# Kernel optimization log

Measured on AMD Instinct MI355X. Metric: run time of the kernel, lower is better.

The kernel has to match this reference:

```python
import jax, jax.numpy as jnp
import numpy as np

B, TQ, TV, D = 8, 2048, 2048, 128
NEG = 1e9  # keras Attention uses additive -1e9 masking for fp32


def setup_inputs() -> dict:
    key = jax.random.key(0)
    kq, kv, kk, kmq, kmv = jax.random.split(key, 5)
    q = jax.random.normal(kq, (B, TQ, D), dtype=jnp.float32)
    v = jax.random.normal(kv, (B, TV, D), dtype=jnp.float32)
    k = jax.random.normal(kk, (B, TV, D), dtype=jnp.float32)
    # learned scalar scale from use_scale=True, initialized to ones
    scale = jnp.ones((), dtype=jnp.float32)
    mask_q = jax.random.randint(kmq, (B, TQ), 0, 2) > 0
    mask_v = jax.random.randint(kmv, (B, TV), 0, 2) > 0
    return {"q": q, "v": v, "k": k, "scale": scale, "mask_q": mask_q, "mask_v": mask_v}


def reference(q, v, k, scale, mask_q, mask_v):
    # scores: [B, Tq, Tv]
    scores = scale * jnp.einsum('bqd,bkd->bqk', q, k)
    # key/value mask: additive -1e9 on masked positions (keras semantics)
    scores = scores - NEG * (1.0 - mask_v[:, None, :].astype(scores.dtype))
    weights = jax.nn.softmax(scores, axis=-1)
    out = jnp.einsum('bqk,bkd->bqd', weights, v)
    # query mask zeroes out masked query rows
    out = out * mask_q[:, :, None].astype(out.dtype)
    return out
```

## Files before the change

kernel.cpp:

```cpp
#include <hip/hip_runtime.h>
#include <cstddef>

#define NB 8
#define TQ 2048
#define TV 2048
#define DD 128
#define KVT 32
#define NWV 4
#define CHW (TV / NWV)
#define NT  (CHW / KVT)

typedef _Float16 f16x8 __attribute__((ext_vector_type(8)));
typedef _Float16 f16x4 __attribute__((ext_vector_type(4)));
typedef float f32x4 __attribute__((ext_vector_type(4)));

template <int CTRL>
__device__ __forceinline__ float dpp_mov(float x) {
  return __builtin_bit_cast(float,
      __builtin_amdgcn_update_dpp(0, __builtin_bit_cast(int, x), CTRL, 0xF, 0xF, true));
}
__device__ __forceinline__ float rowmax16(float x) {
  x = fmaxf(x, dpp_mov<0x128>(x));
  x = fmaxf(x, dpp_mov<0x124>(x));
  x = fmaxf(x, dpp_mov<0x122>(x));
  x = fmaxf(x, dpp_mov<0x121>(x));
  return x;
}

__global__ __launch_bounds__(256) void prepass_kernel(
    const float* __restrict__ q, const float* __restrict__ k,
    const float* __restrict__ v, const float* __restrict__ scale_p,
    _Float16* __restrict__ qh, _Float16* __restrict__ kh2, _Float16* __restrict__ vt2)
{
  __shared__ _Float16 tlds[32 * 34];
  const int tid = threadIdx.x;
  const int bid = blockIdx.x;
  if (bid < 2048) {
    const float sc = scale_p[0];
    size_t idx = (size_t)bid * 256 + tid;
    float4 x = ((const float4*)q)[idx];
    f16x4 h; h[0] = (_Float16)(sc * x.x); h[1] = (_Float16)(sc * x.y);
    h[2] = (_Float16)(sc * x.z); h[3] = (_Float16)(sc * x.w);
    ((f16x4*)qh)[idx] = h;
  } else if (bid < 2048 + 512) {
    int tb = bid - 2048;
    int b = tb >> 6, kt = tb & 63;
    int row = tid >> 3, d0 = (tid & 7) * 4;
    const float* src = k + ((size_t)(b * TV + kt * 32 + row)) * DD;
    _Float16* dst = kh2 + ((size_t)(b * 64 + kt)) * 4096;
#pragma unroll
    for (int it = 0; it < 4; ++it) {
      float4 x = *(const float4*)(src + it * 32 + d0);
      f16x4 h; h[0] = (_Float16)x.x; h[1] = (_Float16)x.y;
      h[2] = (_Float16)x.z; h[3] = (_Float16)x.w;
      *(f16x4*)(dst + it * 1024 + row * 32 + d0) = h;
    }
  } else {
    int tb = bid - 2048 - 512;
    int b = tb >> 8, rem = tb & 255;
    int kt = rem >> 2, dt = rem & 3;
    int r = tid >> 3, c0 = (tid & 7) * 4;
    float4 x = *(const float4*)&v[((size_t)b * TV + kt * 32 + r) * DD + dt * 32 + c0];
    tlds[(c0 + 0) * 34 + r] = (_Float16)x.x;
    tlds[(c0 + 1) * 34 + r] = (_Float16)x.y;
    tlds[(c0 + 2) * 34 + r] = (_Float16)x.z;
    tlds[(c0 + 3) * 34 + r] = (_Float16)x.w;
    __syncthreads();
    int dl = tid >> 3, k0 = (tid & 7) * 4;
    f16x4 h;
#pragma unroll
    for (int i = 0; i < 4; ++i) h[i] = tlds[dl * 34 + k0 + i];
    size_t eidx = (((size_t)b * 64 + kt) * 128 + (dt * 32 + dl)) * 32 + k0;
    *(f16x4*)&vt2[eidx] = h;
  }
}

__global__ __launch_bounds__(256, 2) void attn_main(
    const _Float16* __restrict__ qh, const _Float16* __restrict__ kh2,
    const _Float16* __restrict__ vt2,
    const int* __restrict__ mask_q, const int* __restrict__ mask_v,
    float* __restrict__ out)
{
  __shared__ __align__(16) _Float16 plds_all[NWV][2][16 * 40];
  __shared__ __align__(16) float osh[32 * 132];
  __shared__ float msh[NWV][32], lsh[NWV][32];

  const int tid = threadIdx.x;
  const int w = tid >> 6;
  const int lane = tid & 63;
  const int l15 = lane & 15, lg = lane >> 4;

  const int b = blockIdx.x & 7;
  const int qg = blockIdx.x >> 3;
  const int qbase = qg * 32;

  const _Float16* qhb = qh + ((size_t)b * TQ + qbase) * DD;
  const _Float16* ktiles = kh2 + (size_t)b * 64 * 4096;
  const _Float16* vtiles = vt2 + (size_t)b * 64 * 4096;
  const int* mvb = mask_v + b * TV;

  f16x8 qf[2][4];
#pragma unroll
  for (int rb = 0; rb < 2; ++rb)
#pragma unroll
    for (int kc = 0; kc < 4; ++kc)
      qf[rb][kc] = *(const f16x8*)(qhb + (size_t)(rb * 16 + l15) * DD + kc * 32 + lg * 8);

  f16x8 vones;
#pragma unroll
  for (int j = 0; j < 8; ++j) vones[j] = (_Float16)1.f;

  f32x4 acc[2][8];
  f32x4 accl[2];
#pragma unroll
  for (int rb = 0; rb < 2; ++rb) {
    accl[rb] = (f32x4){0.f, 0.f, 0.f, 0.f};
#pragma unroll
    for (int ct = 0; ct < 8; ++ct) acc[rb][ct] = (f32x4){0.f, 0.f, 0.f, 0.f};
  }
  float m[2][4];
#pragma unroll
  for (int rb = 0; rb < 2; ++rb)
#pragma unroll
    for (int r = 0; r < 4; ++r) m[rb][r] = -3.0e38f;

  const int tbase = w * NT;

  f16x8 ka[8], kb[8];

  {
    const _Float16* kt0 = ktiles + (size_t)tbase * 4096;
#pragma unroll
    for (int kc = 0; kc < 4; ++kc) {
      ka[2 * kc]     = *(const f16x8*)(kt0 + kc * 1024 + l15 * 32 + lg * 8);
      ka[2 * kc + 1] = *(const f16x8*)(kt0 + kc * 1024 + (16 + l15) * 32 + lg * 8);
    }
  }

  auto step = [&](int tile, f16x8 (&kcur)[8], f16x8 (&kpre)[8], int tilep) {
    const _Float16* ktbp = ktiles + (size_t)tilep * 4096;
#pragma unroll
    for (int kc = 0; kc < 4; ++kc) {
      kpre[2 * kc]     = *(const f16x8*)(ktbp + kc * 1024 + l15 * 32 + lg * 8);
      kpre[2 * kc + 1] = *(const f16x8*)(ktbp + kc * 1024 + (16 + l15) * 32 + lg * 8);
    }
    const _Float16* vtb = vtiles + (size_t)tile * 4096;
    f16x8 vfr[8];
#pragma unroll
    for (int ct = 0; ct < 8; ++ct)
      vfr[ct] = *(const f16x8*)(vtb + (ct * 16 + l15) * 32 + lg * 8);
    const int kt = tile * KVT;
    const float a0 = (mvb[kt + l15]      != 0) ? 0.f : -1e9f;
    const float a1 = (mvb[kt + 16 + l15] != 0) ? 0.f : -1e9f;

    f32x4 s[2][2];
    s[0][0] = (f32x4){0,0,0,0}; s[0][1] = (f32x4){0,0,0,0};
    s[1][0] = (f32x4){0,0,0,0}; s[1][1] = (f32x4){0,0,0,0};
    __builtin_amdgcn_s_setprio(1);
#pragma unroll
    for (int kc = 0; kc < 4; ++kc) {
      s[0][0] = __builtin_amdgcn_mfma_f32_16x16x32_f16(qf[0][kc], kcur[2*kc],   s[0][0], 0, 0, 0);
      s[1][0] = __builtin_amdgcn_mfma_f32_16x16x32_f16(qf[1][kc], kcur[2*kc],   s[1][0], 0, 0, 0);
      s[0][1] = __builtin_amdgcn_mfma_f32_16x16x32_f16(qf[0][kc], kcur[2*kc+1], s[0][1], 0, 0, 0);
      s[1][1] = __builtin_amdgcn_mfma_f32_16x16x32_f16(qf[1][kc], kcur[2*kc+1], s[1][1], 0, 0, 0);
    }
    __builtin_amdgcn_s_setprio(0);

    f16x8 pa[2];
#pragma unroll
    for (int rb = 0; rb < 2; ++rb) {
      float pmx[4];
      bool grow = false;
#pragma unroll
      for (int r = 0; r < 4; ++r) {
        s[rb][0][r] += a0;
        s[rb][1][r] += a1;
        pmx[r] = rowmax16(fmaxf(s[rb][0][r], s[rb][1][r]));
        grow = grow || (pmx[r] > m[rb][r] + 8.f);
      }
      if (__any(grow)) {
        f32x4 alv;
#pragma unroll
        for (int r = 0; r < 4; ++r) {
          float mn = fmaxf(m[rb][r], pmx[r]);
          alv[r] = __expf(m[rb][r] - mn);
          m[rb][r] = mn;
        }
        accl[rb] *= alv;
#pragma unroll
        for (int ct = 0; ct < 8; ++ct) acc[rb][ct] *= alv;
      }
      _Float16* pl = plds_all[w][rb];
#pragma unroll
      for (int r = 0; r < 4; ++r) {
        float p0 = __expf(s[rb][0][r] - m[rb][r]);
        float p1 = __expf(s[rb][1][r] - m[rb][r]);
        int row = lg * 4 + r;
        pl[row * 40 + l15]      = (_Float16)p0;
        pl[row * 40 + 16 + l15] = (_Float16)p1;
      }
      pa[rb] = *(const f16x8*)(pl + l15 * 40 + lg * 8);
    }

    __builtin_amdgcn_s_setprio(1);
#pragma unroll
    for (int ct = 0; ct < 8; ++ct) {
      acc[0][ct] = __builtin_amdgcn_mfma_f32_16x16x32_f16(pa[0], vfr[ct], acc[0][ct], 0, 0, 0);
      acc[1][ct] = __builtin_amdgcn_mfma_f32_16x16x32_f16(pa[1], vfr[ct], acc[1][ct], 0, 0, 0);
    }
    accl[0] = __builtin_amdgcn_mfma_f32_16x16x32_f16(pa[0], vones, accl[0], 0, 0, 0);
    accl[1] = __builtin_amdgcn_mfma_f32_16x16x32_f16(pa[1], vones, accl[1], 0, 0, 0);
    __builtin_amdgcn_s_setprio(0);
  };

#pragma unroll 1
  for (int t2 = 0; t2 < NT; t2 += 2) {
    step(tbase + t2,     ka, kb, tbase + t2 + 1);
    step(tbase + t2 + 1, kb, ka, (t2 + 2 < NT) ? (tbase + t2 + 2) : (tbase + t2 + 1));
  }

  if (l15 == 0) {
#pragma unroll
    for (int rb = 0; rb < 2; ++rb)
#pragma unroll
      for (int r = 0; r < 4; ++r) {
        msh[w][rb * 16 + lg * 4 + r] = m[rb][r];
        lsh[w][rb * 16 + lg * 4 + r] = accl[rb][r];
      }
  }
  __syncthreads();

  float coef[2][4];
#pragma unroll
  for (int rb = 0; rb < 2; ++rb)
#pragma unroll
    for (int r = 0; r < 4; ++r) {
      int row = rb * 16 + lg * 4 + r;
      float mstar = msh[0][row];
#pragma unroll
      for (int wv = 1; wv < NWV; ++wv) mstar = fmaxf(mstar, msh[wv][row]);
      coef[rb][r] = __expf(m[rb][r] - mstar);
    }

#pragma unroll
  for (int wv = 0; wv < NWV; ++wv) {
    if (w == wv) {
#pragma unroll
      for (int rb = 0; rb < 2; ++rb)
#pragma unroll
        for (int ct = 0; ct < 8; ++ct)
#pragma unroll
          for (int r = 0; r < 4; ++r) {
            int idx = (rb * 16 + lg * 4 + r) * 132 + ct * 16 + l15;
            float val = coef[rb][r] * acc[rb][ct][r];
            if (wv == 0) osh[idx] = val; else osh[idx] += val;
          }
    }
    __syncthreads();
  }

  {
    const int row = tid >> 3;
    const int cg = (tid & 7) * 16;
    float mstar = msh[0][row];
#pragma unroll
    for (int wv = 1; wv < NWV; ++wv) mstar = fmaxf(mstar, msh[wv][row]);
    float lstar = 0.f;
#pragma unroll
    for (int wv = 0; wv < NWV; ++wv)
      lstar += __expf(msh[wv][row] - mstar) * lsh[wv][row];
    const int qr = qbase + row;
    const float f = ((mask_q[(size_t)b * TQ + qr] != 0) ? 1.f : 0.f) / lstar;
    float* orow = out + ((size_t)b * TQ + qr) * DD + cg;
#pragma unroll
    for (int i4 = 0; i4 < 4; ++i4) {
      float4 p = *(float4*)&osh[row * 132 + cg + i4 * 4];
      float4 o; o.x = p.x * f; o.y = p.y * f; o.z = p.z * f; o.w = p.w * f;
      *(float4*)(orow + i4 * 4) = o;
    }
  }
}

__global__ __launch_bounds__(64, 4) void attn_f32_kernel(
    const float* __restrict__ q, const float* __restrict__ v,
    const float* __restrict__ k, const float* __restrict__ scale_p,
    const int* __restrict__ mask_q, const int* __restrict__ mask_v,
    float* __restrict__ out)
{
  __shared__ __align__(16) _Float16 plds[16 * 40];
  const int lane = threadIdx.x & 63;
  const int l15 = lane & 15, lg = lane >> 4;
  const int qblocks = TQ / 16;
  const int b = blockIdx.x / qblocks, qb = blockIdx.x % qblocks;
  const int qbase = qb * 16;
  const float scale = scale_p[0];
  const float* qp = q + ((size_t)b * TQ + qbase) * DD;
  const float* kbase = k + (size_t)b * TV * DD;
  const float* vbase = v + (size_t)b * TV * DD;
  const int* mvb = mask_v + b * TV;
  f16x8 qf[4];
#pragma unroll
  for (int kc = 0; kc < 4; ++kc) {
    float4 a = *(const float4*)(qp + (size_t)l15 * DD + kc * 32 + lg * 8);
    float4 bb = *(const float4*)(qp + (size_t)l15 * DD + kc * 32 + lg * 8 + 4);
    f16x8 h; h[0]=(_Float16)a.x;h[1]=(_Float16)a.y;h[2]=(_Float16)a.z;h[3]=(_Float16)a.w;
    h[4]=(_Float16)bb.x;h[5]=(_Float16)bb.y;h[6]=(_Float16)bb.z;h[7]=(_Float16)bb.w;
    qf[kc]=h;
  }
  f32x4 acc[8];
#pragma unroll
  for (int i = 0; i < 8; ++i) acc[i] = (f32x4){0.f,0.f,0.f,0.f};
  float m[4], lsum[4];
#pragma unroll
  for (int r = 0; r < 4; ++r) { m[r] = -3.0e38f; lsum[r] = 0.f; }
  for (int kt = 0; kt < TV; kt += KVT) {
    f32x4 s0 = {0,0,0,0}, s1 = {0,0,0,0};
#pragma unroll
    for (int kc = 0; kc < 4; ++kc) {
      const float* kp0 = kbase + (size_t)(kt + l15) * DD + kc * 32 + lg * 8;
      float4 a = *(const float4*)kp0; float4 bb = *(const float4*)(kp0 + 4);
      f16x8 kf0; kf0[0]=(_Float16)a.x;kf0[1]=(_Float16)a.y;kf0[2]=(_Float16)a.z;kf0[3]=(_Float16)a.w;
      kf0[4]=(_Float16)bb.x;kf0[5]=(_Float16)bb.y;kf0[6]=(_Float16)bb.z;kf0[7]=(_Float16)bb.w;
      s0 = __builtin_amdgcn_mfma_f32_16x16x32_f16(qf[kc], kf0, s0, 0, 0, 0);
      const float* kp1 = kbase + (size_t)(kt + 16 + l15) * DD + kc * 32 + lg * 8;
      a = *(const float4*)kp1; bb = *(const float4*)(kp1 + 4);
      f16x8 kf1; kf1[0]=(_Float16)a.x;kf1[1]=(_Float16)a.y;kf1[2]=(_Float16)a.z;kf1[3]=(_Float16)a.w;
      kf1[4]=(_Float16)bb.x;kf1[5]=(_Float16)bb.y;kf1[6]=(_Float16)bb.z;kf1[7]=(_Float16)bb.w;
      s1 = __builtin_amdgcn_mfma_f32_16x16x32_f16(qf[kc], kf1, s1, 0, 0, 0);
    }
    const float a0 = (mvb[kt + l15] != 0) ? 0.f : -1e9f;
    const float a1 = (mvb[kt + 16 + l15] != 0) ? 0.f : -1e9f;
    float pmx[4];
#pragma unroll
    for (int r = 0; r < 4; ++r) {
      s0[r] = s0[r] * scale + a0; s1[r] = s1[r] * scale + a1;
      pmx[r] = fmaxf(s0[r], s1[r]);
    }
#pragma unroll
    for (int off = 1; off < 16; off <<= 1)
#pragma unroll
      for (int r = 0; r < 4; ++r) pmx[r] = fmaxf(pmx[r], __shfl_xor(pmx[r], off, 64));
    float al[4], ps[4];
#pragma unroll
    for (int r = 0; r < 4; ++r) {
      float mn = fmaxf(m[r], pmx[r]);
      al[r] = __expf(m[r] - mn); m[r] = mn;
      float p0 = __expf(s0[r] - mn), p1 = __expf(s1[r] - mn);
      ps[r] = p0 + p1;
      int row = lg * 4 + r;
      plds[row * 40 + l15] = (_Float16)p0;
      plds[row * 40 + 16 + l15] = (_Float16)p1;
    }
#pragma unroll
    for (int off = 1; off < 16; off <<= 1)
#pragma unroll
      for (int r = 0; r < 4; ++r) ps[r] += __shfl_xor(ps[r], off, 64);
#pragma unroll
    for (int r = 0; r < 4; ++r) {
      lsum[r] = lsum[r] * al[r] + ps[r];
#pragma unroll
      for (int ct = 0; ct < 8; ++ct) acc[ct][r] *= al[r];
    }
    f16x8 pa = *(const f16x8*)&plds[l15 * 40 + lg * 8];
#pragma unroll
    for (int ct = 0; ct < 8; ++ct) {
      const float* vp = vbase + (size_t)(kt + lg * 8) * DD + ct * 16 + l15;
      f16x8 vfx;
#pragma unroll
      for (int j = 0; j < 8; ++j) vfx[j] = (_Float16)vp[(size_t)j * DD];
      acc[ct] = __builtin_amdgcn_mfma_f32_16x16x32_f16(pa, vfx, acc[ct], 0, 0, 0);
    }
  }
  const int* mqb = mask_q + b * TQ;
#pragma unroll
  for (int r = 0; r < 4; ++r) {
    int row = lg * 4 + r;
    int qr = qbase + row;
    float f = ((mqb[qr] != 0) ? 1.f : 0.f) / lsum[r];
    float* orow = out + ((size_t)b * TQ + qr) * DD;
#pragma unroll
    for (int ct = 0; ct < 8; ++ct) orow[ct * 16 + l15] = acc[ct][r] * f;
  }
}

extern "C" void kernel_launch(void* const* d_in, const int* in_sizes, int n_in,
                              void* d_out, int out_size, void* d_ws, size_t ws_size,
                              hipStream_t stream) {
  const float* q      = (const float*)d_in[0];
  const float* v      = (const float*)d_in[1];
  const float* k      = (const float*)d_in[2];
  const float* scale  = (const float*)d_in[3];
  const int*   mask_q = (const int*)d_in[4];
  const int*   mask_v = (const int*)d_in[5];
  float* out = (float*)d_out;

  const size_t need = 3ull * NB * TV * DD * sizeof(_Float16);
  if (ws_size >= need) {
    _Float16* qh  = (_Float16*)d_ws;
    _Float16* kh2 = qh + (size_t)NB * TQ * DD;
    _Float16* vt2 = kh2 + (size_t)NB * TV * DD;
    hipLaunchKernelGGL(prepass_kernel, dim3(2048 + 512 + 2048), dim3(256), 0, stream,
                       q, k, v, scale, qh, kh2, vt2);
    hipLaunchKernelGGL(attn_main, dim3(NB * (TQ / 32)), dim3(256), 0, stream,
                       qh, kh2, vt2, mask_q, mask_v, out);
  } else {
    hipLaunchKernelGGL(attn_f32_kernel, dim3(NB * (TQ / 16)), dim3(64), 0, stream,
                       q, v, k, scale, mask_q, mask_v, out);
  }
}
```

Before: 56.55 us.

## Fuse Q conversion into attention kernel, use exp2 softmax and precomputed mask biases

Drops the Q fp32-to-fp16 prepass and has the attention kernel load fp32 Q and convert it, with the scale and log2(e) folded in, so the qh workspace round trip goes away. Softmax switches from __expf to the hardware exp2 builtin. Mask biases are precomputed per tile as packed fp16 values in registers. The lazy-rescale row max is now taken only when a rescale triggers, using a larger threshold, and the K/V loop is fully unrolled with single-buffered prefetch of the next K and V. The larger rescale threshold and the fp16 -60000 mask bias change numeric headroom, and full unrolling raises register pressure.

After: 56.38 us. About the same (-0.3%).

```diff
diff --git a/kernel.cpp b/kernel.cpp
--- a/kernel.cpp
+++ b/kernel.cpp
@@ -9,10 +9,15 @@
 #define NWV 4
 #define CHW (TV / NWV)
 #define NT  (CHW / KVT)
+#define LOG2E 1.4426950408889634f
 
 typedef _Float16 f16x8 __attribute__((ext_vector_type(8)));
 typedef _Float16 f16x4 __attribute__((ext_vector_type(4)));
 typedef float f32x4 __attribute__((ext_vector_type(4)));
+
+__device__ __forceinline__ float fast_exp2(float x) {
+  return __builtin_amdgcn_exp2f(x);
+}
 
 template <int CTRL>
 __device__ __forceinline__ float dpp_mov(float x) {
@@ -28,23 +33,14 @@
 }
 
 __global__ __launch_bounds__(256) void prepass_kernel(
-    const float* __restrict__ q, const float* __restrict__ k,
-    const float* __restrict__ v, const float* __restrict__ scale_p,
-    _Float16* __restrict__ qh, _Float16* __restrict__ kh2, _Float16* __restrict__ vt2)
+    const float* __restrict__ k, const float* __restrict__ v,
+    _Float16* __restrict__ kh2, _Float16* __restrict__ vt2)
 {
   __shared__ _Float16 tlds[32 * 34];
   const int tid = threadIdx.x;
   const int bid = blockIdx.x;
-  if (bid < 2048) {
-    const float sc = scale_p[0];
-    size_t idx = (size_t)bid * 256 + tid;
-    float4 x = ((const float4*)q)[idx];
-    f16x4 h; h[0] = (_Float16)(sc * x.x); h[1] = (_Float16)(sc * x.y);
-    h[2] = (_Float16)(sc * x.z); h[3] = (_Float16)(sc * x.w);
-    ((f16x4*)qh)[idx] = h;
-  } else if (bid < 2048 + 512) {
-    int tb = bid - 2048;
-    int b = tb >> 6, kt = tb & 63;
+  if (bid < 512) {
+    int b = bid >> 6, kt = bid & 63;
     int row = tid >> 3, d0 = (tid & 7) * 4;
     const float* src = k + ((size_t)(b * TV + kt * 32 + row)) * DD;
     _Float16* dst = kh2 + ((size_t)(b * 64 + kt)) * 4096;
@@ -56,7 +52,7 @@
       *(f16x4*)(dst + it * 1024 + row * 32 + d0) = h;
     }
   } else {
-    int tb = bid - 2048 - 512;
+    int tb = bid - 512;
     int b = tb >> 8, rem = tb & 255;
     int kt = rem >> 2, dt = rem & 3;
     int r = tid >> 3, c0 = (tid & 7) * 4;
@@ -76,8 +72,8 @@
 }
 
 __global__ __launch_bounds__(256, 2) void attn_main(
-    const _Float16* __restrict__ qh, const _Float16* __restrict__ kh2,
-    const _Float16* __restrict__ vt2,
+    const float* __restrict__ q, const float* __restrict__ scale_p,
+    const _Float16* __restrict__ kh2, const _Float16* __restrict__ vt2,
     const int* __restrict__ mask_q, const int* __restrict__ mask_v,
     float* __restrict__ out)
 {
@@ -93,18 +89,37 @@
   const int b = blockIdx.x & 7;
   const int qg = blockIdx.x >> 3;
   const int qbase = qg * 32;
-
-  const _Float16* qhb = qh + ((size_t)b * TQ + qbase) * DD;
+  const int kv0 = w * CHW;
+
   const _Float16* ktiles = kh2 + (size_t)b * 64 * 4096;
   const _Float16* vtiles = vt2 + (size_t)b * 64 * 4096;
   const int* mvb = mask_v + b * TV;
 
+  const float sc2 = scale_p[0] * LOG2E;
   f16x8 qf[2][4];
 #pragma unroll
   for (int rb = 0; rb < 2; ++rb)
 #pragma unroll
-    for (int kc = 0; kc < 4; ++kc)
-      qf[rb][kc] = *(const f16x8*)(qhb + (size_t)(rb * 16 + l15) * DD + kc * 32 + lg * 8);
+    for (int kc = 0; kc < 4; ++kc) {
+      const float* qp = q + ((size_t)b * TQ + qbase + rb * 16 + l15) * DD + kc * 32 + lg * 8;
+      float4 xa = *(const float4*)qp;
+      float4 xb = *(const float4*)(qp + 4);
+      f16x8 h;
+      h[0] = (_Float16)(sc2 * xa.x); h[1] = (_Float16)(sc2 * xa.y);
+      h[2] = (_Float16)(sc2 * xa.z); h[3] = (_Float16)(sc2 * xa.w);
+      h[4] = (_Float16)(sc2 * xb.x); h[5] = (_Float16)(sc2 * xb.y);
+      h[6] = (_Float16)(sc2 * xb.z); h[7] = (_Float16)(sc2 * xb.w);
+      qf[rb][kc] = h;
+    }
+
+  const unsigned short HBIAS = __builtin_bit_cast(unsigned short, (_Float16)(-60000.0f));
+  unsigned mbp[NT];
+#pragma unroll
+  for (int t = 0; t < NT; ++t) {
+    unsigned h0 = (mvb[kv0 + t * KVT + l15]      != 0) ? 0u : (unsigned)HBIAS;
+    unsigned h1 = (mvb[kv0 + t * KVT + 16 + l15] != 0) ? 0u : (unsigned)HBIAS;
+    mbp[t] = h0 | (h1 << 16);
+  }
 
   f16x8 vones;
 #pragma unroll
@@ -126,32 +141,23 @@
 
   const int tbase = w * NT;
 
-  f16x8 ka[8], kb[8];
-
+  f16x8 kbuf[8], vbuf[8];
   {
-    const _Float16* kt0 = ktiles + (size_t)tbase * 4096;
+    const _Float16* ktb = ktiles + (size_t)tbase * 4096;
 #pragma unroll
     for (int kc = 0; kc < 4; ++kc) {
-      ka[2 * kc]     = *(const f16x8*)(kt0 + kc * 1024 + l15 * 32 + lg * 8);
-      ka[2 * kc + 1] = *(const f16x8*)(kt0 + kc * 1024 + (16 + l15) * 32 + lg * 8);
-    }
-  }
-
-  auto step = [&](int tile, f16x8 (&kcur)[8], f16x8 (&kpre)[8], int tilep) {
-    const _Float16* ktbp = ktiles + (size_t)tilep * 4096;
-#pragma unroll
-    for (int kc = 0; kc < 4; ++kc) {
-      kpre[2 * kc]     = *(const f16x8*)(ktbp + kc * 1024 + l15 * 32 + lg * 8);
-      kpre[2 * kc + 1] = *(const f16x8*)(ktbp + kc * 1024 + (16 + l15) * 32 + lg * 8);
-    }
-    const _Float16* vtb = vtiles + (size_t)tile * 4096;
-    f16x8 vfr[8];
+      kbuf[2 * kc]     = *(const f16x8*)(ktb + kc * 1024 + l15 * 32 + lg * 8);
+      kbuf[2 * kc + 1] = *(const f16x8*)(ktb + kc * 1024 + (16 + l15) * 32 + lg * 8);
+    }
+    const _Float16* vtb = vtiles + (size_t)tbase * 4096;
 #pragma unroll
     for (int ct = 0; ct < 8; ++ct)
-      vfr[ct] = *(const f16x8*)(vtb + (ct * 16 + l15) * 32 + lg * 8);
-    const int kt = tile * KVT;
-    const float a0 = (mvb[kt + l15]      != 0) ? 0.f : -1e9f;
-    const float a1 = (mvb[kt + 16 + l15] != 0) ? 0.f : -1e9f;
+      vbuf[ct] = *(const f16x8*)(vtb + (ct * 16 + l15) * 32 + lg * 8);
+  }
+
+#pragma unroll
+  for (int t = 0; t < NT; ++t) {
+    const int tile = tbase + t;
 
     f32x4 s[2][2];
     s[0][0] = (f32x4){0,0,0,0}; s[0][1] = (f32x4){0,0,0,0};
@@ -159,31 +165,43 @@
     __builtin_amdgcn_s_setprio(1);
 #pragma unroll
     for (int kc = 0; kc < 4; ++kc) {
-      s[0][0] = __builtin_amdgcn_mfma_f32_16x16x32_f16(qf[0][kc], kcur[2*kc],   s[0][0], 0, 0, 0);
-      s[1][0] = __builtin_amdgcn_mfma_f32_16x16x32_f16(qf[1][kc], kcur[2*kc],   s[1][0], 0, 0, 0);
-      s[0][1] = __builtin_amdgcn_mfma_f32_16x16x32_f16(qf[0][kc], kcur[2*kc+1], s[0][1], 0, 0, 0);
-      s[1][1] = __builtin_amdgcn_mfma_f32_16x16x32_f16(qf[1][kc], kcur[2*kc+1], s[1][1], 0, 0, 0);
+      s[0][0] = __builtin_amdgcn_mfma_f32_16x16x32_f16(qf[0][kc], kbuf[2*kc],   s[0][0], 0, 0, 0);
+      s[1][0] = __builtin_amdgcn_mfma_f32_16x16x32_f16(qf[1][kc], kbuf[2*kc],   s[1][0], 0, 0, 0);
+      s[0][1] = __builtin_amdgcn_mfma_f32_16x16x32_f16(qf[0][kc], kbuf[2*kc+1], s[0][1], 0, 0, 0);
+      s[1][1] = __builtin_amdgcn_mfma_f32_16x16x32_f16(qf[1][kc], kbuf[2*kc+1], s[1][1], 0, 0, 0);
     }
     __builtin_amdgcn_s_setprio(0);
 
+    if (t + 1 < NT) {
+      const _Float16* ktb = ktiles + (size_t)(tile + 1) * 4096;
+#pragma unroll
+      for (int kc = 0; kc < 4; ++kc) {
+        kbuf[2 * kc]     = *(const f16x8*)(ktb + kc * 1024 + l15 * 32 + lg * 8);
+        kbuf[2 * kc + 1] = *(const f16x8*)(ktb + kc * 1024 + (16 + l15) * 32 + lg * 8);
+      }
+    }
+
+    const float b0 = (float)__builtin_bit_cast(_Float16, (unsigned short)(mbp[t] & 0xFFFFu));
+    const float b1 = (float)__builtin_bit_cast(_Float16, (unsigned short)(mbp[t] >> 16));
     f16x8 pa[2];
 #pragma unroll
     for (int rb = 0; rb < 2; ++rb) {
-      float pmx[4];
+      float plm[4];
       bool grow = false;
 #pragma unroll
       for (int r = 0; r < 4; ++r) {
-        s[rb][0][r] += a0;
-        s[rb][1][r] += a1;
-        pmx[r] = rowmax16(fmaxf(s[rb][0][r], s[rb][1][r]));
-        grow = grow || (pmx[r] > m[rb][r] + 8.f);
+        s[rb][0][r] += b0;
+        s[rb][1][r] += b1;
+        plm[r] = fmaxf(s[rb][0][r], s[rb][1][r]);
+        grow = grow || (plm[r] > m[rb][r] + 11.5f);
       }
       if (__any(grow)) {
         f32x4 alv;
 #pragma unroll
         for (int r = 0; r < 4; ++r) {
-          float mn = fmaxf(m[rb][r], pmx[r]);
-          alv[r] = __expf(m[rb][r] - mn);
+          float pmx = rowmax16(plm[r]);
+          float mn = fmaxf(m[rb][r], pmx);
+          alv[r] = fast_exp2(m[rb][r] - mn);
           m[rb][r] = mn;
         }
         accl[rb] *= alv;
@@ -193,8 +211,8 @@
       _Float16* pl = plds_all[w][rb];
 #pragma unroll
       for (int r = 0; r < 4; ++r) {
-        float p0 = __expf(s[rb][0][r] - m[rb][r]);
-        float p1 = __expf(s[rb][1][r] - m[rb][r]);
+        float p0 = fast_exp2(s[rb][0][r] - m[rb][r]);
+        float p1 = fast_exp2(s[rb][1][r] - m[rb][r]);
         int row = lg * 4 + r;
         pl[row * 40 + l15]      = (_Float16)p0;
         pl[row * 40 + 16 + l15] = (_Float16)p1;
@@ -205,18 +223,19 @@
     __builtin_amdgcn_s_setprio(1);
 #pragma unroll
     for (int ct = 0; ct < 8; ++ct) {
-      acc[0][ct] = __builtin_amdgcn_mfma_f32_16x16x32_f16(pa[0], vfr[ct], acc[0][ct], 0, 0, 0);
-      acc[1][ct] = __builtin_amdgcn_mfma_f32_16x16x32_f16(pa[1], vfr[ct], acc[1][ct], 0, 0, 0);
+      acc[0][ct] = __builtin_amdgcn_mfma_f32_16x16x32_f16(pa[0], vbuf[ct], acc[0][ct], 0, 0, 0);
+      acc[1][ct] = __builtin_amdgcn_mfma_f32_16x16x32_f16(pa[1], vbuf[ct], acc[1][ct], 0, 0, 0);
     }
     accl[0] = __builtin_amdgcn_mfma_f32_16x16x32_f16(pa[0], vones, accl[0], 0, 0, 0);
     accl[1] = __builtin_amdgcn_mfma_f32_16x16x32_f16(pa[1], vones, accl[1], 0, 0, 0);
     __builtin_amdgcn_s_setprio(0);
-  };
-
-#pragma unroll 1
-  for (int t2 = 0; t2 < NT; t2 += 2) {
-    step(tbase + t2,     ka, kb, tbase + t2 + 1);
-    step(tbase + t2 + 1, kb, ka, (t2 + 2 < NT) ? (tbase + t2 + 2) : (tbase + t2 + 1));
+
+    if (t + 1 < NT) {
+      const _Float16* vtb = vtiles + (size_t)(tile + 1) * 4096;
+#pragma unroll
+      for (int ct = 0; ct < 8; ++ct)
+        vbuf[ct] = *(const f16x8*)(vtb + (ct * 16 + l15) * 32 + lg * 8);
+    }
   }
 
   if (l15 == 0) {
@@ -239,7 +258,7 @@
       float mstar = msh[0][row];
 #pragma unroll
       for (int wv = 1; wv < NWV; ++wv) mstar = fmaxf(mstar, msh[wv][row]);
-      coef[rb][r] = __expf(m[rb][r] - mstar);
+      coef[rb][r] = fast_exp2(m[rb][r] - mstar);
     }
 
 #pragma unroll
@@ -268,7 +287,7 @@
     float lstar = 0.f;
 #pragma unroll
     for (int wv = 0; wv < NWV; ++wv)
-      lstar += __expf(msh[wv][row] - mstar) * lsh[wv][row];
+      lstar += fast_exp2(msh[wv][row] - mstar) * lsh[wv][row];
     const int qr = qbase + row;
     const float f = ((mask_q[(size_t)b * TQ + qr] != 0) ? 1.f : 0.f) / lstar;
     float* orow = out + ((size_t)b * TQ + qr) * DD + cg;
@@ -394,15 +413,14 @@
   const int*   mask_v = (const int*)d_in[5];
   float* out = (float*)d_out;
 
-  const size_t need = 3ull * NB * TV * DD * sizeof(_Float16);
+  const size_t need = 2ull * NB * TV * DD * sizeof(_Float16);
   if (ws_size >= need) {
-    _Float16* qh  = (_Float16*)d_ws;
-    _Float16* kh2 = qh + (size_t)NB * TQ * DD;
+    _Float16* kh2 = (_Float16*)d_ws;
     _Float16* vt2 = kh2 + (size_t)NB * TV * DD;
-    hipLaunchKernelGGL(prepass_kernel, dim3(2048 + 512 + 2048), dim3(256), 0, stream,
-                       q, k, v, scale, qh, kh2, vt2);
+    hipLaunchKernelGGL(prepass_kernel, dim3(512 + 2048), dim3(256), 0, stream,
+                       k, v, kh2, vt2);
     hipLaunchKernelGGL(attn_main, dim3(NB * (TQ / 32)), dim3(256), 0, stream,
-                       qh, kh2, vt2, mask_q, mask_v, out);
+                       q, scale, kh2, vt2, mask_q, mask_v, out);
   } else {
     hipLaunchKernelGGL(attn_f32_kernel, dim3(NB * (TQ / 16)), dim3(64), 0, stream,
                        q, v, k, scale, mask_q, mask_v, out);
```
